# Kernel tuning notes

Hardware: AMD Instinct MI355X
Metric: run time of the kernel (lower is better)

Reference implementation:

```python
import jax, jax.numpy as jnp
import numpy as np

C = 512
GROUPS = 8
EPS = 1e-5


def setup_inputs() -> dict:
    key = jax.random.key(0)
    ks = jax.random.split(key, 7)
    b, c, h, w = 32, C, 32, 32
    x = jax.random.normal(ks[0], (b, c, h, w), dtype=jnp.float32)
    norm_gamma = jnp.ones((c,), dtype=jnp.float32)
    norm_beta = jnp.zeros((c,), dtype=jnp.float32)
    # 1x1 convs == per-pixel linear layers; store as [out, in] matrices
    qkv_w = jax.random.normal(ks[1], (3 * c, c), dtype=jnp.float32) * (1.0 / np.sqrt(c))
    qkv_b = jnp.zeros((3 * c,), dtype=jnp.float32)
    out_w = jax.random.normal(ks[2], (c, c), dtype=jnp.float32) * (1.0 / np.sqrt(c))
    out_b = jnp.zeros((c,), dtype=jnp.float32)
    return {"x": x, "norm_gamma": norm_gamma, "norm_beta": norm_beta,
            "qkv_w": qkv_w, "qkv_b": qkv_b, "out_w": out_w, "out_b": out_b}


def group_norm(x, gamma, beta):
    b, c, h, w = x.shape
    xg = x.reshape(b, GROUPS, c // GROUPS, h, w)
    mean = jnp.mean(xg, axis=(2, 3, 4), keepdims=True)
    var = jnp.var(xg, axis=(2, 3, 4), keepdims=True)
    xg = (xg - mean) * jax.lax.rsqrt(var + EPS)
    x = xg.reshape(b, c, h, w)
    return x * gamma[None, :, None, None] + beta[None, :, None, None]


def reference(x, norm_gamma, norm_beta, qkv_w, qkv_b, out_w, out_b):
    b, c, h, w = x.shape
    xn = group_norm(x, norm_gamma, norm_beta)
    # 1x1 conv: [b,c,h,w] -> [b,3c,h,w]
    qkv = jnp.einsum('oc,bchw->bohw', qkv_w, xn) + qkv_b[None, :, None, None]
    q, k, v = jnp.split(qkv.reshape(b, 3 * c, h * w), 3, axis=1)  # each [b,c,hw]
    scale = c ** (-0.5)
    attn = jnp.einsum('bci,bcj->bij', q, k) * scale  # [b, hw, hw]
    attn = jax.nn.softmax(attn, axis=-1)
    out = jnp.einsum('bij,bcj->bci', attn, v).reshape(b, c, h, w)
    out = jnp.einsum('oc,bchw->bohw', out_w, out) + out_b[None, :, None, None]
    return x + out
```

## Files before the change

kernel.cpp:

```cpp
#include <hip/hip_runtime.h>

#define HW 1024
#define CD 512

typedef __bf16 bf16x8 __attribute__((ext_vector_type(8)));
typedef float f32x4 __attribute__((ext_vector_type(4)));

__device__ __forceinline__ unsigned short f2bf(float f) {
    unsigned int u = __float_as_uint(f);
    u += 0x7fff + ((u >> 16) & 1);
    return (unsigned short)(u >> 16);
}
__device__ __forceinline__ float bf2f(unsigned short h) {
    return __uint_as_float((unsigned)h << 16);
}

#define AS1(p) ((__attribute__((address_space(1))) void*)(p))
#define AS3(p) ((__attribute__((address_space(3))) void*)(p))
#define GLD16(gp, lp) __builtin_amdgcn_global_load_lds(AS1(gp), AS3(lp), 16, 0, 0)

__global__ __launch_bounds__(256)
void gn_stats(const float* __restrict__ x, float* __restrict__ mean, float* __restrict__ rstd) {
    int bg = blockIdx.x;
    const float4* p4 = (const float4*)(x + (size_t)bg * 65536);
    int tid = threadIdx.x;
    float s = 0.f, ss = 0.f;
#pragma unroll 8
    for (int it = 0; it < 64; ++it) {
        float4 v = p4[tid + it * 256];
        s  += v.x + v.y + v.z + v.w;
        ss += v.x * v.x + v.y * v.y + v.z * v.z + v.w * v.w;
    }
#pragma unroll
    for (int d = 32; d > 0; d >>= 1) { s += __shfl_down(s, d); ss += __shfl_down(ss, d); }
    __shared__ float ls[4], lss[4];
    if ((tid & 63) == 0) { ls[tid >> 6] = s; lss[tid >> 6] = ss; }
    __syncthreads();
    if (tid == 0) {
        float S = ls[0] + ls[1] + ls[2] + ls[3];
        float SS = lss[0] + lss[1] + lss[2] + lss[3];
        float m = S * (1.f / 65536.f);
        float v = SS * (1.f / 65536.f) - m * m;
        mean[bg] = m;
        rstd[bg] = rsqrtf(v + 1e-5f);
    }
}

__global__ __launch_bounds__(256)
void gn_norm_t(const float* __restrict__ x, const float* __restrict__ mean, const float* __restrict__ rstd,
               const float* __restrict__ gamma, const float* __restrict__ beta,
               unsigned short* __restrict__ xnT) {
    __shared__ unsigned short tile[64][72];
    int i0 = blockIdx.x * 64, c0 = blockIdx.y * 64, b = blockIdx.z;
    float m = mean[b * 8 + blockIdx.y];
    float r = rstd[b * 8 + blockIdx.y];
    int tid = threadIdx.x;
    int tr = tid >> 4, tc = (tid & 15) * 4;
    const float* xb = x + ((size_t)b * CD + c0) * HW + i0;
#pragma unroll
    for (int p = 0; p < 4; ++p) {
        int c = tr + p * 16;
        float g = gamma[c0 + c] * r;
        float bb = beta[c0 + c] - m * g;
        float4 v = *(const float4*)(xb + (size_t)c * HW + tc);
        tile[c][tc + 0] = f2bf(v.x * g + bb);
        tile[c][tc + 1] = f2bf(v.y * g + bb);
        tile[c][tc + 2] = f2bf(v.z * g + bb);
        tile[c][tc + 3] = f2bf(v.w * g + bb);
    }
    __syncthreads();
    unsigned short* ob = xnT + ((size_t)b * HW + i0) * CD + c0;
#pragma unroll
    for (int p = 0; p < 4; ++p) {
        int ir = tr + p * 16;
        ushort4 u;
        u.x = tile[tc + 0][ir];
        u.y = tile[tc + 1][ir];
        u.z = tile[tc + 2][ir];
        u.w = tile[tc + 3][ir];
        *(ushort4*)(ob + (size_t)ir * CD + tc) = u;
    }
}

__global__ __launch_bounds__(256)
void cvt_bf16(const float* __restrict__ src, unsigned short* __restrict__ dst) {
    int i = blockIdx.x * 256 + threadIdx.x;
    float4 v = ((const float4*)src)[i];
    ushort4 u;
    u.x = f2bf(v.x); u.y = f2bf(v.y); u.z = f2bf(v.z); u.w = f2bf(v.w);
    ((ushort4*)dst)[i] = u;
}

__global__ __launch_bounds__(256)
void w2_kernel(const float* __restrict__ out_w, const float* __restrict__ qkv_w,
               const float* __restrict__ qkv_b, unsigned short* __restrict__ w2,
               float* __restrict__ bias2) {
    int bo = blockIdx.x;
    int tid = threadIdx.x;
    int c2 = tid * 2;
    const float* wv = qkv_w + (size_t)1024 * CD;
    const float* bv = qkv_b + 1024;
    float acc0[2] = {}, acc1[2] = {}, b2[2] = {};
    for (int t = 0; t < CD; ++t) {
        float2 v = *(const float2*)(wv + (size_t)t * CD + c2);
        float bvt = bv[t];
#pragma unroll
        for (int r = 0; r < 2; ++r) {
            float ow = out_w[(size_t)(bo * 2 + r) * CD + t];
            acc0[r] += ow * v.x;
            acc1[r] += ow * v.y;
            b2[r]   += ow * bvt;
        }
    }
#pragma unroll
    for (int r = 0; r < 2; ++r) {
        unsigned int pack = (unsigned int)f2bf(acc0[r]) | ((unsigned int)f2bf(acc1[r]) << 16);
        *(unsigned int*)(w2 + (size_t)(bo * 2 + r) * CD + c2) = pack;
        if (tid == 0) bias2[bo * 2 + r] = b2[r];
    }
}

template<int EPI>
__global__ __launch_bounds__(256, 2)
void gemm_bt(const unsigned short* __restrict__ A, const unsigned short* __restrict__ B,
             void* __restrict__ Cv, const float* __restrict__ bias,
             const float* __restrict__ resid,
             int M, int N, int K, long long sA, long long sB, long long sC, long long sR) {
    unsigned nx = gridDim.x, ny = gridDim.y;
    unsigned lin = blockIdx.x + nx * (blockIdx.y + ny * blockIdx.z);
    unsigned nwg = nx * ny * gridDim.z;
    unsigned work = (lin & 7) * (nwg >> 3) + (lin >> 3);
    unsigned bx = work % nx; work /= nx;
    unsigned by = work % ny;
    unsigned bz = work / ny;

    A += (size_t)bz * sA;
    B += (size_t)bz * sB;
    int m0 = by * 128, n0 = bx * 128;

    __shared__ unsigned short lA[128 * 64];
    __shared__ unsigned short lB[128 * 64];

    int tid = threadIdx.x;
    int lane = tid & 63;
    int wr = (tid >> 6) >> 1, wc = (tid >> 6) & 1;

    f32x4 acc[4][4] = {};

    int strow[4], stcol[4];
#pragma unroll
    for (int s = 0; s < 4; ++s) {
        int row = (s * 256 + tid) >> 3;
        int g = (tid & 7) ^ (row & 7);
        strow[s] = row;
        stcol[s] = g * 8;
    }

    for (int k0 = 0; k0 < K; k0 += 64) {
#pragma unroll
        for (int s = 0; s < 4; ++s) {
            GLD16(A + (size_t)(m0 + strow[s]) * K + k0 + stcol[s], lA + (size_t)(s * 256 + tid) * 8);
            GLD16(B + (size_t)(n0 + strow[s]) * K + k0 + stcol[s], lB + (size_t)(s * 256 + tid) * 8);
        }
        __syncthreads();
#pragma unroll
        for (int kk = 0; kk < 64; kk += 32) {
            bf16x8 af[4], bfr[4];
#pragma unroll
            for (int m = 0; m < 4; ++m) {
                int row = wr * 64 + m * 16 + (lane & 15);
                int off = (row * 128 + (kk + (lane >> 4) * 8) * 2) ^ ((row & 7) << 4);
                af[m] = *(const bf16x8*)((const char*)lA + off);
            }
#pragma unroll
            for (int n = 0; n < 4; ++n) {
                int row = wc * 64 + n * 16 + (lane & 15);
                int off = (row * 128 + (kk + (lane >> 4) * 8) * 2) ^ ((row & 7) << 4);
                bfr[n] = *(const bf16x8*)((const char*)lB + off);
            }
#pragma unroll
            for (int m = 0; m < 4; ++m)
#pragma unroll
                for (int n = 0; n < 4; ++n)
                    acc[m][n] = __builtin_amdgcn_mfma_f32_16x16x32_bf16(af[m], bfr[n], acc[m][n], 0, 0, 0);
        }
        __syncthreads();
    }

    int rl = (lane >> 4) * 4;
    int cl = lane & 15;
    if (EPI == 2) {
        float* Cf = (float*)Cv + (size_t)bz * sC;
        const float* Rs = resid + (size_t)bz * sR;
#pragma unroll
        for (int m = 0; m < 4; ++m)
#pragma unroll
            for (int n = 0; n < 4; ++n) {
                int gm = m0 + wr * 64 + m * 16 + rl;
                int gn = n0 + wc * 64 + n * 16 + cl;
#pragma unroll
                for (int rg = 0; rg < 4; ++rg) {
                    size_t off = (size_t)(gm + rg) * N + gn;
                    Cf[off] = acc[m][n][rg] + bias[gm + rg] + Rs[off];
                }
            }
    } else {
        unsigned short* Cb = (unsigned short*)Cv + (size_t)bz * sC;
#pragma unroll
        for (int m = 0; m < 4; ++m)
#pragma unroll
            for (int n = 0; n < 4; ++n) {
                int gm = m0 + wr * 64 + m * 16 + rl;
                int gn = n0 + wc * 64 + n * 16 + cl;
#pragma unroll
                for (int rg = 0; rg < 4; ++rg) {
                    float v = acc[m][n][rg] + (EPI == 0 ? bias[gn] : bias[gm + rg]);
                    Cb[(size_t)(gm + rg) * N + gn] = f2bf(v);
                }
            }
    }
}

__global__ __launch_bounds__(256, 2)
void scores_gemm(const unsigned short* __restrict__ qk, unsigned short* __restrict__ S,
                 float* __restrict__ tmax, float* __restrict__ tsum) {
    unsigned lin = blockIdx.x + 8u * (blockIdx.y + 8u * blockIdx.z);
    unsigned work = (lin & 7) * 256 + (lin >> 3);
    unsigned bx = work & 7; work >>= 3;
    unsigned by = work & 7;
    unsigned bz = work >> 3;
    const unsigned short* qkb = qk + (size_t)bz * HW * HW;
    int m0 = by * 128, n0 = bx * 128;

    __shared__ unsigned short lA[128 * 64];
    __shared__ unsigned short lB[128 * 64];
    __shared__ float redm[2][128];
    __shared__ float reds[2][128];

    int tid = threadIdx.x, lane = tid & 63;
    int wr = (tid >> 6) >> 1, wc = (tid >> 6) & 1;

    f32x4 acc[4][4] = {};
    int strow[4], stcol[4];
#pragma unroll
    for (int s = 0; s < 4; ++s) {
        int row = (s * 256 + tid) >> 3;
        int g = (tid & 7) ^ (row & 7);
        strow[s] = row;
        stcol[s] = g * 8;
    }

    for (int k0 = 0; k0 < CD; k0 += 64) {
#pragma unroll
        for (int s = 0; s < 4; ++s) {
            GLD16(qkb + (size_t)(m0 + strow[s]) * HW + k0 + stcol[s], lA + (size_t)(s * 256 + tid) * 8);
            GLD16(qkb + (size_t)(n0 + strow[s]) * HW + 512 + k0 + stcol[s], lB + (size_t)(s * 256 + tid) * 8);
        }
        __syncthreads();
#pragma unroll
        for (int kk = 0; kk < 64; kk += 32) {
            bf16x8 af[4], bfr[4];
#pragma unroll
            for (int m = 0; m < 4; ++m) {
                int row = wr * 64 + m * 16 + (lane & 15);
                int off = (row * 128 + (kk + (lane >> 4) * 8) * 2) ^ ((row & 7) << 4);
                af[m] = *(const bf16x8*)((const char*)lA + off);
            }
#pragma unroll
            for (int n = 0; n < 4; ++n) {
                int row = wc * 64 + n * 16 + (lane & 15);
                int off = (row * 128 + (kk + (lane >> 4) * 8) * 2) ^ ((row & 7) << 4);
                bfr[n] = *(const bf16x8*)((const char*)lB + off);
            }
#pragma unroll
            for (int m = 0; m < 4; ++m)
#pragma unroll
                for (int n = 0; n < 4; ++n)
                    acc[m][n] = __builtin_amdgcn_mfma_f32_16x16x32_bf16(af[m], bfr[n], acc[m][n], 0, 0, 0);
        }
        __syncthreads();
    }

    const float SL2E = 0.044194173824159216f * 1.4426950408889634f;
#pragma unroll
    for (int m = 0; m < 4; ++m)
#pragma unroll
        for (int n = 0; n < 4; ++n) acc[m][n] *= SL2E;

    int rl = (lane >> 4) * 4;
    int cl = lane & 15;

    float mr[4][4];
#pragma unroll
    for (int m = 0; m < 4; ++m)
#pragma unroll
        for (int rg = 0; rg < 4; ++rg)
            mr[m][rg] = fmaxf(fmaxf(acc[m][0][rg], acc[m][1][rg]),
                              fmaxf(acc[m][2][rg], acc[m][3][rg]));
#pragma unroll
    for (int d = 1; d < 16; d <<= 1)
#pragma unroll
        for (int m = 0; m < 4; ++m)
#pragma unroll
            for (int rg = 0; rg < 4; ++rg) mr[m][rg] = fmaxf(mr[m][rg], __shfl_xor(mr[m][rg], d));
    if ((lane & 15) == 0)
#pragma unroll
        for (int m = 0; m < 4; ++m)
#pragma unroll
            for (int rg = 0; rg < 4; ++rg) redm[wc][wr * 64 + m * 16 + rl + rg] = mr[m][rg];
    __syncthreads();
    float Mt[4][4];
#pragma unroll
    for (int m = 0; m < 4; ++m)
#pragma unroll
        for (int rg = 0; rg < 4; ++rg) {
            int row = wr * 64 + m * 16 + rl + rg;
            Mt[m][rg] = fmaxf(redm[0][row], redm[1][row]);
        }

    float sr[4][4] = {};
#pragma unroll
    for (int m = 0; m < 4; ++m)
#pragma unroll
        for (int n = 0; n < 4; ++n)
#pragma unroll
            for (int rg = 0; rg < 4; ++rg) sr[m][rg] += exp2f(acc[m][n][rg] - Mt[m][rg]);
#pragma unroll
    for (int d = 1; d < 16; d <<= 1)
#pragma unroll
        for (int m = 0; m < 4; ++m)
#pragma unroll
            for (int rg = 0; rg < 4; ++rg) sr[m][rg] += __shfl_xor(sr[m][rg], d);
    if ((lane & 15) == 0)
#pragma unroll
        for (int m = 0; m < 4; ++m)
#pragma unroll
            for (int rg = 0; rg < 4; ++rg) reds[wc][wr * 64 + m * 16 + rl + rg] = sr[m][rg];
    __syncthreads();

    if (tid < 128) {
        float M = fmaxf(redm[0][tid], redm[1][tid]);
        float Z = reds[0][tid] + reds[1][tid];
        size_t o = ((size_t)bz * 8 + bx) * HW + m0 + tid;
        tmax[o] = M;
        tsum[o] = Z;
    }

    unsigned short* Sb = S + (size_t)bz * HW * HW;
#pragma unroll
    for (int m = 0; m < 4; ++m)
#pragma unroll
        for (int n = 0; n < 4; ++n) {
            int gm = m0 + wr * 64 + m * 16 + rl;
            int gn = n0 + wc * 64 + n * 16 + cl;
#pragma unroll
            for (int rg = 0; rg < 4; ++rg)
                Sb[(size_t)(gm + rg) * HW + gn] = f2bf(acc[m][n][rg]);
        }
}

__global__ __launch_bounds__(256)
void row_reduce(const float* __restrict__ tmax, const float* __restrict__ tsum,
                float* __restrict__ rowM, float* __restrict__ rowRZ) {
    int r = blockIdx.x * 256 + threadIdx.x;
    int b = r >> 10, i = r & 1023;
    const float* tm = tmax + (size_t)b * 8 * HW + i;
    const float* ts = tsum + (size_t)b * 8 * HW + i;
    float M = -1e30f;
#pragma unroll
    for (int jt = 0; jt < 8; ++jt) M = fmaxf(M, tm[(size_t)jt * HW]);
    float Z = 0.f;
#pragma unroll
    for (int jt = 0; jt < 8; ++jt) Z += ts[(size_t)jt * HW] * exp2f(tm[(size_t)jt * HW] - M);
    rowM[r] = M;
    rowRZ[r] = 1.0f / Z;
}

__global__ __launch_bounds__(256)
void pnorm(unsigned short* __restrict__ SP, const float* __restrict__ rowM,
           const float* __restrict__ rowRZ) {
    size_t gid = (size_t)blockIdx.x * 256 + threadIdx.x;
    int row = (int)(gid >> 7);
    float M = rowM[row], rz = rowRZ[row];
    uint4 v = ((const uint4*)SP)[gid];
    unsigned* w = (unsigned*)&v;
#pragma unroll
    for (int k = 0; k < 4; ++k) {
        float a = bf2f((unsigned short)(w[k] & 0xffff));
        float c = bf2f((unsigned short)(w[k] >> 16));
        a = exp2f(a - M) * rz;
        c = exp2f(c - M) * rz;
        w[k] = (unsigned)f2bf(a) | ((unsigned)f2bf(c) << 16);
    }
    ((uint4*)SP)[gid] = v;
}

extern "C" void kernel_launch(void* const* d_in, const int* in_sizes, int n_in,
                              void* d_out, int out_size, void* d_ws, size_t ws_size,
                              hipStream_t stream) {
    const float* x      = (const float*)d_in[0];
    const float* gamma  = (const float*)d_in[1];
    const float* beta   = (const float*)d_in[2];
    const float* qkv_w  = (const float*)d_in[3];
    const float* qkv_b  = (const float*)d_in[4];
    const float* out_w  = (const float*)d_in[5];
    const float* out_b  = (const float*)d_in[6];

    char* ws = (char*)d_ws;
    unsigned short* xnT  = (unsigned short*)ws;
    unsigned short* SP   = (unsigned short*)ws;
    unsigned short* vpr  = (unsigned short*)(ws + 67108864);
    unsigned short* wqk  = (unsigned short*)(ws + 100663296);
    unsigned short* w2   = (unsigned short*)(ws + 101711872);
    float* bias2         = (float*)(ws + 102236160);
    float* meanp         = (float*)(ws + 102238208);
    float* rstdp         = (float*)(ws + 102239232);
    float* tmaxp         = (float*)(ws + 102760448);
    float* tsump         = (float*)(ws + 103809024);
    float* rowMp         = (float*)(ws + 104857600);
    float* rowRZp        = (float*)(ws + 104988672);

    unsigned short* qkT = (unsigned short*)d_out;
    float* outF = (float*)d_out;

    gn_stats<<<256, 256, 0, stream>>>(x, meanp, rstdp);
    gn_norm_t<<<dim3(16, 8, 32), 256, 0, stream>>>(x, meanp, rstdp, gamma, beta, xnT);
    cvt_bf16<<<512, 256, 0, stream>>>(qkv_w, wqk);
    w2_kernel<<<256, 256, 0, stream>>>(out_w, qkv_w, qkv_b, w2, bias2);

    gemm_bt<0><<<dim3(8, 8, 32), 256, 0, stream>>>(xnT, wqk, qkT, qkv_b, nullptr,
        1024, 1024, 512, 1024LL * 512, 0, 1024LL * 1024, 0);
    gemm_bt<1><<<dim3(8, 4, 32), 256, 0, stream>>>(w2, xnT, vpr, bias2, nullptr,
        512, 1024, 512, 0, 1024LL * 512, 512LL * 1024, 0);
    scores_gemm<<<dim3(8, 8, 32), 256, 0, stream>>>(qkT, SP, tmaxp, tsump);
    row_reduce<<<128, 256, 0, stream>>>(tmaxp, tsump, rowMp, rowRZp);
    pnorm<<<16384, 256, 0, stream>>>(SP, rowMp, rowRZp);
    gemm_bt<2><<<dim3(8, 4, 32), 256, 0, stream>>>(vpr, SP, outF, out_b, x,
        512, 1024, 1024, 512LL * 1024, 1024LL * 1024, 512LL * 1024, 512LL * 1024);
    (void)in_sizes; (void)n_in; (void)out_size; (void)ws_size;
}
```

Baseline: 247.9 us.

## Fold Wq^T Wk into one matrix and split attention into two batch halves

Precomputes Wqk = Wk^T Wq and a key-side bias vector, so the QKV projection emits a single 512-wide T1 = xn·Wqk^T per pixel and the scores GEMM multiplies T1 against xnT directly. This halves the first projection GEMM's output width and the score GEMM's operand traffic. It drops the per-query bias terms, which cancel in the softmax. The attention stages now run in two halves of 16 batches so that SP and T1 fit in smaller workspace and output regions. exp2f is also replaced with the hardware exp2 intrinsic, which may lose some accuracy and adds launches.

```diff
diff --git a/kernel.cpp b/kernel.cpp
--- a/kernel.cpp
+++ b/kernel.cpp
@@ -83,12 +83,31 @@
 }
 
 __global__ __launch_bounds__(256)
-void cvt_bf16(const float* __restrict__ src, unsigned short* __restrict__ dst) {
-    int i = blockIdx.x * 256 + threadIdx.x;
-    float4 v = ((const float4*)src)[i];
-    ushort4 u;
-    u.x = f2bf(v.x); u.y = f2bf(v.y); u.z = f2bf(v.z); u.w = f2bf(v.w);
-    ((ushort4*)dst)[i] = u;
+void wqk_kernel(const float* __restrict__ qkv_w, const float* __restrict__ qkv_b,
+                unsigned short* __restrict__ wqkT, float* __restrict__ g) {
+    int bo = blockIdx.x;
+    int tid = threadIdx.x;
+    int c2 = tid * 2;
+    const float* wq = qkv_w;
+    const float* wk = qkv_w + (size_t)512 * CD;
+    float acc0[2] = {}, acc1[2] = {}, gg[2] = {};
+    for (int o = 0; o < CD; ++o) {
+        float2 v = *(const float2*)(wq + (size_t)o * CD + c2);
+        float bqo = qkv_b[o];
+#pragma unroll
+        for (int r = 0; r < 2; ++r) {
+            float wkd = wk[(size_t)o * CD + bo * 2 + r];
+            acc0[r] += wkd * v.x;
+            acc1[r] += wkd * v.y;
+            gg[r]   += wkd * bqo;
+        }
+    }
+#pragma unroll
+    for (int r = 0; r < 2; ++r) {
+        unsigned pack = (unsigned)f2bf(acc0[r]) | ((unsigned)f2bf(acc1[r]) << 16);
+        *(unsigned*)(wqkT + (size_t)(bo * 2 + r) * CD + c2) = pack;
+        if (tid == 0) g[bo * 2 + r] = gg[r];
+    }
 }
 
 __global__ __launch_bounds__(256)
@@ -222,14 +241,18 @@
 }
 
 __global__ __launch_bounds__(256, 2)
-void scores_gemm(const unsigned short* __restrict__ qk, unsigned short* __restrict__ S,
-                 float* __restrict__ tmax, float* __restrict__ tsum) {
-    unsigned lin = blockIdx.x + 8u * (blockIdx.y + 8u * blockIdx.z);
-    unsigned work = (lin & 7) * 256 + (lin >> 3);
-    unsigned bx = work & 7; work >>= 3;
-    unsigned by = work & 7;
-    unsigned bz = work >> 3;
-    const unsigned short* qkb = qk + (size_t)bz * HW * HW;
+void scores_gemm(const unsigned short* __restrict__ T1, const unsigned short* __restrict__ xnT,
+                 unsigned short* __restrict__ S, float* __restrict__ tmax, float* __restrict__ tsum) {
+    unsigned nx = gridDim.x, ny = gridDim.y;
+    unsigned lin = blockIdx.x + nx * (blockIdx.y + ny * blockIdx.z);
+    unsigned nwg = nx * ny * gridDim.z;
+    unsigned work = (lin & 7) * (nwg >> 3) + (lin >> 3);
+    unsigned bx = work % nx; work /= nx;
+    unsigned by = work % ny;
+    unsigned bz = work / ny;
+
+    const unsigned short* Ab = T1 + (size_t)bz * HW * CD;
+    const unsigned short* Bb = xnT + (size_t)bz * HW * CD;
     int m0 = by * 128, n0 = bx * 128;
 
     __shared__ unsigned short lA[128 * 64];
@@ -253,8 +276,8 @@
     for (int k0 = 0; k0 < CD; k0 += 64) {
 #pragma unroll
         for (int s = 0; s < 4; ++s) {
-            GLD16(qkb + (size_t)(m0 + strow[s]) * HW + k0 + stcol[s], lA + (size_t)(s * 256 + tid) * 8);
-            GLD16(qkb + (size_t)(n0 + strow[s]) * HW + 512 + k0 + stcol[s], lB + (size_t)(s * 256 + tid) * 8);
+            GLD16(Ab + (size_t)(m0 + strow[s]) * CD + k0 + stcol[s], lA + (size_t)(s * 256 + tid) * 8);
+            GLD16(Bb + (size_t)(n0 + strow[s]) * CD + k0 + stcol[s], lB + (size_t)(s * 256 + tid) * 8);
         }
         __syncthreads();
 #pragma unroll
@@ -324,7 +347,7 @@
 #pragma unroll
         for (int n = 0; n < 4; ++n)
 #pragma unroll
-            for (int rg = 0; rg < 4; ++rg) sr[m][rg] += exp2f(acc[m][n][rg] - Mt[m][rg]);
+            for (int rg = 0; rg < 4; ++rg) sr[m][rg] += __builtin_amdgcn_exp2f(acc[m][n][rg] - Mt[m][rg]);
 #pragma unroll
     for (int d = 1; d < 16; d <<= 1)
 #pragma unroll
@@ -371,7 +394,7 @@
     for (int jt = 0; jt < 8; ++jt) M = fmaxf(M, tm[(size_t)jt * HW]);
     float Z = 0.f;
 #pragma unroll
-    for (int jt = 0; jt < 8; ++jt) Z += ts[(size_t)jt * HW] * exp2f(tm[(size_t)jt * HW] - M);
+    for (int jt = 0; jt < 8; ++jt) Z += ts[(size_t)jt * HW] * __builtin_amdgcn_exp2f(tm[(size_t)jt * HW] - M);
     rowM[r] = M;
     rowRZ[r] = 1.0f / Z;
 }
@@ -388,8 +411,8 @@
     for (int k = 0; k < 4; ++k) {
         float a = bf2f((unsigned short)(w[k] & 0xffff));
         float c = bf2f((unsigned short)(w[k] >> 16));
-        a = exp2f(a - M) * rz;
-        c = exp2f(c - M) * rz;
+        a = __builtin_amdgcn_exp2f(a - M) * rz;
+        c = __builtin_amdgcn_exp2f(c - M) * rz;
         w[k] = (unsigned)f2bf(a) | ((unsigned)f2bf(c) << 16);
     }
     ((uint4*)SP)[gid] = v;
@@ -408,34 +431,47 @@
 
     char* ws = (char*)d_ws;
     unsigned short* xnT  = (unsigned short*)ws;
-    unsigned short* SP   = (unsigned short*)ws;
-    unsigned short* vpr  = (unsigned short*)(ws + 67108864);
-    unsigned short* wqk  = (unsigned short*)(ws + 100663296);
-    unsigned short* w2   = (unsigned short*)(ws + 101711872);
-    float* bias2         = (float*)(ws + 102236160);
-    float* meanp         = (float*)(ws + 102238208);
-    float* rstdp         = (float*)(ws + 102239232);
-    float* tmaxp         = (float*)(ws + 102760448);
-    float* tsump         = (float*)(ws + 103809024);
-    float* rowMp         = (float*)(ws + 104857600);
-    float* rowRZp        = (float*)(ws + 104988672);
-
-    unsigned short* qkT = (unsigned short*)d_out;
+    unsigned short* vpr  = (unsigned short*)(ws + 33554432);
+    unsigned short* SP   = (unsigned short*)(ws + 67108864);
+    unsigned short* wqkT = (unsigned short*)(ws + 100663296);
+    unsigned short* w2   = (unsigned short*)(ws + 101187584);
+    float* gvec          = (float*)(ws + 101711872);
+    float* bias2         = (float*)(ws + 101713920);
+    float* meanp         = (float*)(ws + 101715968);
+    float* rstdp         = (float*)(ws + 101716992);
+    float* tmaxp         = (float*)(ws + 101718016);
+    float* tsump         = (float*)(ws + 102766592);
+    float* rowMp         = (float*)(ws + 103815168);
+    float* rowRZp        = (float*)(ws + 103946240);
+
+    unsigned short* T1 = (unsigned short*)((char*)d_out + 33554432);
     float* outF = (float*)d_out;
 
     gn_stats<<<256, 256, 0, stream>>>(x, meanp, rstdp);
     gn_norm_t<<<dim3(16, 8, 32), 256, 0, stream>>>(x, meanp, rstdp, gamma, beta, xnT);
-    cvt_bf16<<<512, 256, 0, stream>>>(qkv_w, wqk);
+    wqk_kernel<<<256, 256, 0, stream>>>(qkv_w, qkv_b, wqkT, gvec);
     w2_kernel<<<256, 256, 0, stream>>>(out_w, qkv_w, qkv_b, w2, bias2);
 
-    gemm_bt<0><<<dim3(8, 8, 32), 256, 0, stream>>>(xnT, wqk, qkT, qkv_b, nullptr,
-        1024, 1024, 512, 1024LL * 512, 0, 1024LL * 1024, 0);
+    gemm_bt<0><<<dim3(4, 8, 32), 256, 0, stream>>>(xnT, wqkT, T1, gvec, nullptr,
+        1024, 512, 512, 1024LL * 512, 0, 1024LL * 512, 0);
     gemm_bt<1><<<dim3(8, 4, 32), 256, 0, stream>>>(w2, xnT, vpr, bias2, nullptr,
         512, 1024, 512, 0, 1024LL * 512, 512LL * 1024, 0);
-    scores_gemm<<<dim3(8, 8, 32), 256, 0, stream>>>(qkT, SP, tmaxp, tsump);
-    row_reduce<<<128, 256, 0, stream>>>(tmaxp, tsump, rowMp, rowRZp);
-    pnorm<<<16384, 256, 0, stream>>>(SP, rowMp, rowRZp);
-    gemm_bt<2><<<dim3(8, 4, 32), 256, 0, stream>>>(vpr, SP, outF, out_b, x,
-        512, 1024, 1024, 512LL * 1024, 1024LL * 1024, 512LL * 1024, 512LL * 1024);
+
+    for (int h = 0; h < 2; ++h) {
+        const unsigned short* T1h = T1 + (size_t)h * 16 * 1024 * 512;
+        const unsigned short* xh  = xnT + (size_t)h * 16 * 1024 * 512;
+        float* tmaxh  = tmaxp + (size_t)h * 16 * 8 * 1024;
+        float* tsumh  = tsump + (size_t)h * 16 * 8 * 1024;
+        float* rowMh  = rowMp + (size_t)h * 16 * 1024;
+        float* rowRZh = rowRZp + (size_t)h * 16 * 1024;
+
+        scores_gemm<<<dim3(8, 8, 16), 256, 0, stream>>>(T1h, xh, SP, tmaxh, tsumh);
+        row_reduce<<<64, 256, 0, stream>>>(tmaxh, tsumh, rowMh, rowRZh);
+        pnorm<<<8192, 256, 0, stream>>>(SP, rowMh, rowRZh);
+        gemm_bt<2><<<dim3(8, 4, 16), 256, 0, stream>>>(
+            vpr + (size_t)h * 16 * 512 * 1024, SP, outF + (size_t)h * 16 * 512 * 1024,
+            out_b, x + (size_t)h * 16 * 512 * 1024,
+            512, 1024, 1024, 512LL * 1024, 1024LL * 1024, 512LL * 1024, 512LL * 1024);
+    }
     (void)in_sizes; (void)n_in; (void)out_size; (void)ws_size;
 }
```

Measured after the change: 286.1 us. +15.4%, slower.
